# Kernel tuning notes

Hardware: AMD Instinct MI355X
Metric: run time of the kernel (lower is better)

The kernel has to match this reference:

```python
import jax, jax.numpy as jnp
import numpy as np

B, N, HID, LAT, OUT, M = 64, 8192, 96, 1024, 2, 1024
ROWS, COLS, K_HOP = 64, 128, 2
NEG = -10000.0


def _build_hex_neighbors():
    """Hex lattice adjacency + k-hop BFS lookup (mirrors _build_neighbor_lookup)."""
    adj = [[] for _ in range(N)]
    for r in range(ROWS):
        offs = [(-1, -1), (-1, 0), (0, -1), (0, 1), (1, -1), (1, 0)] if r % 2 == 0 \
            else [(-1, 0), (-1, 1), (0, -1), (0, 1), (1, 0), (1, 1)]
        for c in range(COLS):
            u = r * COLS + c
            for dr, dc in offs:
                rr, cc = r + dr, c + dc
                if 0 <= rr < ROWS and 0 <= cc < COLS:
                    adj[u].append(rr * COLS + cc)
    all_nbrs = []
    for node in range(N):
        visited = {node}
        frontier = [node]
        for _ in range(K_HOP):
            nxt = []
            for u in frontier:
                for v in adj[u]:
                    if v not in visited:
                        visited.add(v)
                        nxt.append(v)
            frontier = nxt
        visited.discard(node)
        all_nbrs.append(sorted(visited))
    max_nbrs = max(max(len(n) for n in all_nbrs), 1)
    nbr_idx = np.zeros((N, max_nbrs), dtype=np.int32)
    nbr_cnt = np.zeros((N,), dtype=np.int32)
    for node, nbrs in enumerate(all_nbrs):
        nbr_cnt[node] = len(nbrs)
        if nbrs:
            nbr_idx[node, :len(nbrs)] = np.asarray(nbrs, dtype=np.int32)
    return nbr_idx, nbr_cnt


def setup_inputs() -> dict:
    key = jax.random.key(0)
    ks = jax.random.split(key, 16)
    nbr_idx, nbr_cnt = _build_hex_neighbors()
    # node mask: exactly M masked nodes per sample (static max_masked)
    rng = np.random.default_rng(0)
    mask = np.zeros((B, N), dtype=bool)
    pos = np.argsort(rng.random((B, N)), axis=1)[:, :M]
    mask[np.arange(B)[:, None], pos] = True

    def lin(k, fan_in, fan_out):
        bound = 1.0 / np.sqrt(fan_in)
        kw, kb = jax.random.split(k)
        W = jax.random.uniform(kw, (fan_in, fan_out), jnp.float32, -bound, bound)
        b = jax.random.uniform(kb, (fan_out,), jnp.float32, -bound, bound)
        return W, b

    W_lat, b_lat = lin(ks[0], LAT, HID)
    Wg1, bg1 = lin(ks[1], HID, HID)
    Wg2, bg2 = lin(ks[2], HID, HID)
    Wa, ba = lin(ks[3], HID, 1)
    Wp1, bp1 = lin(ks[4], 2 * HID, HID)
    Wp2, bp2 = lin(ks[5], HID, OUT)
    return {
        "node_features": jax.random.normal(ks[6], (B, N, 2), jnp.float32),
        "latent_token": jax.random.normal(ks[7], (B, LAT), jnp.float32),
        "node_mask": jnp.asarray(mask),
        "nbr_indices": jnp.asarray(nbr_idx),
        "nbr_counts": jnp.asarray(nbr_cnt),
        "max_masked": M,
        "W_lat": W_lat, "b_lat": b_lat,
        "Wg1": Wg1, "bg1": bg1, "Wg2": Wg2, "bg2": bg2,
        "Wa": Wa, "ba": ba,
        "Wp1": Wp1, "bp1": bp1, "Wp2": Wp2, "bp2": bp2,
    }


def _gelu(x):
    return jax.nn.gelu(x, approximate=False)  # torch nn.GELU default (erf)


def reference(node_features, latent_token, node_mask, nbr_indices, nbr_counts,
              max_masked, W_lat, b_lat, Wg1, bg1, Wg2, bg2, Wa, ba,
              Wp1, bp1, Wp2, bp2):
    Bn, Nn, _ = node_features.shape
    H = W_lat.shape[1]
    Kn = nbr_indices.shape[1]
    # latent conditioning + global decoder (use_local_context=False path)
    latent_cond = _gelu(latent_token @ W_lat + b_lat)                  # [B,H]
    x = _gelu(_gelu(latent_cond @ Wg1 + bg1) @ Wg2 + bg2)              # [B,H]
    features = jnp.broadcast_to(x[:, None, :], (Bn, Nn, H))            # [B,N,H]
    # masked node indices per sample, sorted ascending (exactly M per row)
    node_idx = jnp.argsort(jnp.where(node_mask, jnp.arange(Nn)[None, :], Nn),
                           axis=1)[:, :max_masked]                     # [B,M]
    nbrs = nbr_indices[node_idx]                                       # [B,M,K]
    counts = nbr_counts[node_idx]                                      # [B,M]
    in_range = jnp.arange(Kn)[None, None, :] < counts[..., None]
    nbr_is_masked = jnp.take_along_axis(
        node_mask, nbrs.reshape(Bn, -1), axis=1).reshape(Bn, max_masked, Kn)
    valid = in_range & ~nbr_is_masked                                  # [B,M,K]
    nbr_features = jnp.take_along_axis(
        features, nbrs.reshape(Bn, -1, 1), axis=1).reshape(Bn, max_masked, Kn, H)
    logits = jnp.einsum('bmkh,h->bmk', nbr_features, Wa[:, 0]) + ba[0]
    logits = jnp.where(valid, logits, NEG)
    attn = jax.nn.softmax(logits, axis=-1)                             # [B,M,K]
    attended = jnp.einsum('bmk,bmkh->bmh', attn, nbr_features)         # [B,M,H]
    latent_for_masked = jnp.broadcast_to(latent_cond[:, None, :],
                                         (Bn, max_masked, H))
    combined = jnp.concatenate([attended, latent_for_masked], axis=-1)  # [B,M,2H]
    preds = _gelu(combined @ Wp1 + bp1) @ Wp2 + bp2                    # [B,M,OUT]
    valid_mask = jnp.ones((Bn, max_masked), dtype=bool)
    return preds, node_idx, valid_mask
```

## Files before the change

kernel.cpp:

```cpp
#include <hip/hip_runtime.h>

#define B_    64
#define N_    8192
#define HID_  96
#define LAT_  1024
#define OUT_  2
#define M_    1024

#define OFF_IDX (B_ * M_ * OUT_)
#define OFF_VAL (OFF_IDX + B_ * M_)

__device__ __forceinline__ float gelu_erf(float v) {
    return 0.5f * v * (1.0f + erff(v * 0.7071067811865475f));
}

__global__ __launch_bounds__(1024) void fused_kernel(
    const float* __restrict__ latent,
    const void*  __restrict__ mask_raw,
    const float* __restrict__ W_lat, const float* __restrict__ b_lat,
    const float* __restrict__ Wg1,   const float* __restrict__ bg1,
    const float* __restrict__ Wg2,   const float* __restrict__ bg2,
    const float* __restrict__ Wp1,   const float* __restrict__ bp1,
    const float* __restrict__ Wp2,   const float* __restrict__ bp2,
    float* __restrict__ out)
{
    const int tid = threadIdx.x;

    if (blockIdx.x < B_) {
        const int b = blockIdx.x;
        __shared__ float lt[LAT_];
        __shared__ float part[8 * HID_];
        __shared__ float lc[HID_];
        __shared__ float t1[HID_];
        __shared__ float xx[HID_];
        __shared__ float ph[HID_];
        __shared__ float pr[OUT_];

        lt[tid] = latent[b * LAT_ + tid];
        __syncthreads();

        const int h = tid & 127;
        const int s = tid >> 7;

        if (h < HID_) {
            const float* w = W_lat + (size_t)(s * 128) * HID_ + h;
            const int lb = s * 128;
            float a0 = 0.f, a1 = 0.f, a2 = 0.f, a3 = 0.f;
            for (int i = 0; i < 128; i += 4) {
                a0 += lt[lb + i + 0] * w[(i + 0) * HID_];
                a1 += lt[lb + i + 1] * w[(i + 1) * HID_];
                a2 += lt[lb + i + 2] * w[(i + 2) * HID_];
                a3 += lt[lb + i + 3] * w[(i + 3) * HID_];
            }
            part[s * HID_ + h] = (a0 + a1) + (a2 + a3);
        }
        __syncthreads();
        if (tid < HID_) {
            float acc = b_lat[tid];
            for (int q = 0; q < 8; ++q) acc += part[q * HID_ + tid];
            lc[tid] = gelu_erf(acc);
        }
        __syncthreads();

        if (h < HID_) {
            float a = 0.f;
            const int jb = s * 12;
            for (int j = jb; j < jb + 12; ++j) a += lc[j] * Wg1[j * HID_ + h];
            part[s * HID_ + h] = a;
        }
        __syncthreads();
        if (tid < HID_) {
            float acc = bg1[tid];
            for (int q = 0; q < 8; ++q) acc += part[q * HID_ + tid];
            t1[tid] = gelu_erf(acc);
        }
        __syncthreads();

        if (h < HID_) {
            float a = 0.f;
            const int jb = s * 12;
            for (int j = jb; j < jb + 12; ++j) a += t1[j] * Wg2[j * HID_ + h];
            part[s * HID_ + h] = a;
        }
        __syncthreads();
        if (tid < HID_) {
            float acc = bg2[tid];
            for (int q = 0; q < 8; ++q) acc += part[q * HID_ + tid];
            xx[tid] = gelu_erf(acc);
        }
        __syncthreads();

        if (h < HID_) {
            float a = 0.f;
            const int jb = s * 24;
            for (int j = jb; j < jb + 24; ++j) {
                const float v = (j < HID_) ? xx[j] : lc[j - HID_];
                a += v * Wp1[j * HID_ + h];
            }
            part[s * HID_ + h] = a;
        }
        __syncthreads();
        if (tid < HID_) {
            float acc = bp1[tid];
            for (int q = 0; q < 8; ++q) acc += part[q * HID_ + tid];
            ph[tid] = gelu_erf(acc);
        }
        __syncthreads();

        if (tid < 128) {
            const int o = tid >> 6;
            const int lane = tid & 63;
            float a = ph[lane] * Wp2[lane * OUT_ + o];
            if (lane < HID_ - 64) a += ph[lane + 64] * Wp2[(lane + 64) * OUT_ + o];
            for (int d = 32; d > 0; d >>= 1) a += __shfl_down(a, d);
            if (lane == 0) pr[o] = a + bp2[o];
        }
        __syncthreads();

        const float2 p2 = make_float2(pr[0], pr[1]);
        ((float2*)(out + (size_t)b * M_ * OUT_))[tid] = p2;
    } else {
        const int b = blockIdx.x - B_;
        __shared__ int s_cnt;
        __shared__ unsigned s_wcnt[16];

        if (tid == 0) s_cnt = 0;
        __syncthreads();
        const unsigned* mw = (const unsigned*)mask_raw;
        int local = 0;
        for (int w = tid; w < N_ / 4; w += 1024) {
            const unsigned v = mw[w];
            local += ((v & 0xffu) != 0u) + (((v >> 8) & 0xffu) != 0u)
                   + (((v >> 16) & 0xffu) != 0u) + ((v >> 24) != 0u);
        }
        atomicAdd(&s_cnt, local);
        __syncthreads();
        const bool byte_mode = (s_cnt == M_);
        const unsigned char* mb = (const unsigned char*)mask_raw;

        const int lane = tid & 63;
        const int wid  = tid >> 6;
        const unsigned long long lmask = (1ull << lane) - 1ull;
        unsigned base = 0;

        for (int c = 0; c < N_ / 1024; ++c) {
            const int n = c * 1024 + tid;
            const bool m = byte_mode ? (mb[(size_t)b * N_ + n] != 0)
                                     : (mw[(size_t)b * N_ + n] != 0u);
            const unsigned long long bal = __ballot(m);
            const unsigned pre = (unsigned)__popcll(bal & lmask);
            if (lane == 0) s_wcnt[wid] = (unsigned)__popcll(bal);
            __syncthreads();
            unsigned off = 0, tot = 0;
            for (int w = 0; w < 16; ++w) {
                const unsigned cw = s_wcnt[w];
                if (w < wid) off += cw;
                tot += cw;
            }
            if (m) {
                const unsigned pos = base + off + pre;
                if (pos < M_) out[OFF_IDX + b * M_ + pos] = (float)n;
            }
            base += tot;
            __syncthreads();
        }

        out[OFF_VAL + b * M_ + tid] = 1.0f;
    }
}

extern "C" void kernel_launch(void* const* d_in, const int* in_sizes, int n_in,
                              void* d_out, int out_size, void* d_ws, size_t ws_size,
                              hipStream_t stream) {
    const float* latent = (const float*)d_in[1];
    const void*  mask   = d_in[2];
    const float* W_lat  = (const float*)d_in[6];
    const float* b_lat  = (const float*)d_in[7];
    const float* Wg1    = (const float*)d_in[8];
    const float* bg1    = (const float*)d_in[9];
    const float* Wg2    = (const float*)d_in[10];
    const float* bg2    = (const float*)d_in[11];
    const float* Wp1    = (const float*)d_in[14];
    const float* bp1    = (const float*)d_in[15];
    const float* Wp2    = (const float*)d_in[16];
    const float* bp2    = (const float*)d_in[17];
    float* out = (float*)d_out;

    fused_kernel<<<2 * B_, 1024, 0, stream>>>(latent, mask, W_lat, b_lat,
                                              Wg1, bg1, Wg2, bg2,
                                              Wp1, bp1, Wp2, bp2, out);
}
```

Measured before the change: 97.64 us.

## Replace chunked ballot compaction with per-thread 8-element flags and wave scan

The mask-compaction blocks used to walk the row in 8 chunks of 1024, each needing a ballot plus two block barriers. Now each thread loads 8 contiguous mask entries with one vector load, builds a bitmask, and a single wave shuffle scan plus cross-wave prefix gives each thread its output offset. The byte-vs-word mode detection also moves from a shared atomic to a wave reduction. This removes about 16 barriers and the serial chunk loop, at the cost of per-thread serial stores that are no longer coalesced.

Result: no change. 97.35 us (-0.3%).

```diff
diff --git a/kernel.cpp b/kernel.cpp
--- a/kernel.cpp
+++ b/kernel.cpp
@@ -12,6 +12,11 @@
 
 __device__ __forceinline__ float gelu_erf(float v) {
     return 0.5f * v * (1.0f + erff(v * 0.7071067811865475f));
+}
+
+__device__ __forceinline__ int nz_bytes(unsigned v) {
+    return ((v & 0xffu) != 0u) + (((v >> 8) & 0xffu) != 0u)
+         + (((v >> 16) & 0xffu) != 0u) + ((v >> 24) != 0u);
 }
 
 __global__ __launch_bounds__(1024) void fused_kernel(
@@ -24,7 +29,9 @@
     const float* __restrict__ Wp2,   const float* __restrict__ bp2,
     float* __restrict__ out)
 {
-    const int tid = threadIdx.x;
+    const int tid  = threadIdx.x;
+    const int lane = tid & 63;
+    const int wid  = tid >> 6;
 
     if (blockIdx.x < B_) {
         const int b = blockIdx.x;
@@ -109,7 +116,6 @@
 
         if (tid < 128) {
             const int o = tid >> 6;
-            const int lane = tid & 63;
             float a = ph[lane] * Wp2[lane * OUT_ + o];
             if (lane < HID_ - 64) a += ph[lane + 64] * Wp2[(lane + 64) * OUT_ + o];
             for (int d = 32; d > 0; d >>= 1) a += __shfl_down(a, d);
@@ -121,48 +127,52 @@
         ((float2*)(out + (size_t)b * M_ * OUT_))[tid] = p2;
     } else {
         const int b = blockIdx.x - B_;
-        __shared__ int s_cnt;
-        __shared__ unsigned s_wcnt[16];
-
-        if (tid == 0) s_cnt = 0;
-        __syncthreads();
+        __shared__ int      s_det[16];
+        __shared__ unsigned s_wtot[16];
+
         const unsigned* mw = (const unsigned*)mask_raw;
-        int local = 0;
-        for (int w = tid; w < N_ / 4; w += 1024) {
-            const unsigned v = mw[w];
-            local += ((v & 0xffu) != 0u) + (((v >> 8) & 0xffu) != 0u)
-                   + (((v >> 16) & 0xffu) != 0u) + ((v >> 24) != 0u);
-        }
-        atomicAdd(&s_cnt, local);
-        __syncthreads();
-        const bool byte_mode = (s_cnt == M_);
-        const unsigned char* mb = (const unsigned char*)mask_raw;
-
-        const int lane = tid & 63;
-        const int wid  = tid >> 6;
-        const unsigned long long lmask = (1ull << lane) - 1ull;
-        unsigned base = 0;
-
-        for (int c = 0; c < N_ / 1024; ++c) {
-            const int n = c * 1024 + tid;
-            const bool m = byte_mode ? (mb[(size_t)b * N_ + n] != 0)
-                                     : (mw[(size_t)b * N_ + n] != 0u);
-            const unsigned long long bal = __ballot(m);
-            const unsigned pre = (unsigned)__popcll(bal & lmask);
-            if (lane == 0) s_wcnt[wid] = (unsigned)__popcll(bal);
-            __syncthreads();
-            unsigned off = 0, tot = 0;
-            for (int w = 0; w < 16; ++w) {
-                const unsigned cw = s_wcnt[w];
-                if (w < wid) off += cw;
-                tot += cw;
+        {
+            int local = nz_bytes(mw[tid]) + nz_bytes(mw[tid + 1024]);
+            for (int d = 32; d > 0; d >>= 1) local += __shfl_down(local, d);
+            if (lane == 0) s_det[wid] = local;
+        }
+        __syncthreads();
+        int det = 0;
+        for (int w = 0; w < 16; ++w) det += s_det[w];
+        const bool byte_mode = (det == M_);
+
+        unsigned flags = 0;
+        if (byte_mode) {
+            const unsigned long long v =
+                ((const unsigned long long*)mask_raw)[(size_t)b * (N_ / 8) + tid];
+            for (int j = 0; j < 8; ++j)
+                flags |= (((v >> (8 * j)) & 0xffull) != 0ull ? 1u : 0u) << j;
+        } else {
+            const uint4 v0 = ((const uint4*)(mw + (size_t)b * N_))[tid * 2 + 0];
+            const uint4 v1 = ((const uint4*)(mw + (size_t)b * N_))[tid * 2 + 1];
+            flags  = (v0.x != 0u) | ((v0.y != 0u) << 1) | ((v0.z != 0u) << 2)
+                   | ((v0.w != 0u) << 3) | ((v1.x != 0u) << 4)
+                   | ((v1.y != 0u) << 5) | ((v1.z != 0u) << 6)
+                   | ((v1.w != 0u) << 7);
+        }
+        const unsigned cnt = (unsigned)__popc(flags);
+
+        unsigned incl = cnt;
+        for (int d = 1; d < 64; d <<= 1) {
+            const unsigned t = __shfl_up(incl, d);
+            if (lane >= d) incl += t;
+        }
+        if (lane == 63) s_wtot[wid] = incl;
+        __syncthreads();
+        unsigned pos = incl - cnt;
+        for (int w = 0; w < 16; ++w) if (w < wid) pos += s_wtot[w];
+
+        const int nbase = tid * 8;
+        for (int j = 0; j < 8; ++j) {
+            if (flags & (1u << j)) {
+                if (pos < M_) out[OFF_IDX + b * M_ + pos] = (float)(nbase + j);
+                ++pos;
             }
-            if (m) {
-                const unsigned pos = base + off + pre;
-                if (pos < M_) out[OFF_IDX + b * M_ + pos] = (float)n;
-            }
-            base += tot;
-            __syncthreads();
         }
 
         out[OFF_VAL + b * M_ + tid] = 1.0f;
```
